# Kernel optimization log

Hardware: AMD Instinct MI355X
Metric: run time of the kernel (lower is better)

The kernel has to match this reference:

```python
import jax, jax.numpy as jnp
import numpy as np

NEG_INF = -1e9  # stand-in for -INF in masked_fill


def setup_inputs() -> dict:
    key = jax.random.key(0)
    k1, k2, k3 = jax.random.split(key, 3)
    B, S, D = 32, 8192, 512
    query = jax.random.normal(k1, (B, D), dtype=jnp.float32)
    key_t = jax.random.normal(k2, (B, S, D), dtype=jnp.float32)
    value = jax.random.normal(k3, (B, S, D), dtype=jnp.float32)
    mask = jnp.ones((B, 1, S), dtype=jnp.int32)
    return {"query": query, "key": key_t, "value": value, "mask": mask}


def reference(query, key, value, mask):
    # score: [B,1,S] = query [B,D] . key^T [B,D,S]
    score = jnp.einsum('bd,bsd->bs', query, key)[:, None, :]
    score = jnp.where(mask == 0, NEG_INF, score)
    probability = jax.nn.softmax(score, axis=-1)          # [B,1,S]
    out = jnp.einsum('bqs,bsd->bqd', probability, value)  # [B,1,D]
    return out[:, 0, :]                                   # squeeze(1) -> [B,D]
```

## Files before the change

### kernel.cpp

```cpp
#include <hip/hip_runtime.h>
#include <cstddef>

#define BATCH 32
#define SEQ   8192
#define DIM   512
#define NEG_INF_F (-1e9f)

#define NCHUNK 64
#define SCHUNK (SEQ / NCHUNK)

__global__ __launch_bounds__(256) void scores_kernel(
    const float* __restrict__ q, const float* __restrict__ k,
    const int* __restrict__ mask, float* __restrict__ score) {
  const int wave = threadIdx.x >> 6;
  const int lane = threadIdx.x & 63;
  const size_t row = (size_t)blockIdx.x * 4 + wave;
  const int b = (int)(row >> 13);
  const int s = (int)(row & (SEQ - 1));

  const float4* __restrict__ krow = (const float4*)(k + row * DIM);
  const float4* __restrict__ qrow = (const float4*)(q + (size_t)b * DIM);

  const int i0 = lane * 2;
  float4 k0 = krow[i0];
  float4 k1 = krow[i0 + 1];
  float4 q0 = qrow[i0];
  float4 q1 = qrow[i0 + 1];

  float d = k0.x * q0.x + k0.y * q0.y + k0.z * q0.z + k0.w * q0.w
          + k1.x * q1.x + k1.y * q1.y + k1.z * q1.z + k1.w * q1.w;

  #pragma unroll
  for (int off = 32; off > 0; off >>= 1) d += __shfl_down(d, off, 64);

  if (lane == 0) {
    float sc = (mask[(size_t)b * SEQ + s] == 0) ? NEG_INF_F : d;
    score[row] = sc;
  }
}

__global__ __launch_bounds__(256) void softmax_kernel(float* __restrict__ score) {
  __shared__ float red[4];
  const int b = blockIdx.x;
  float* __restrict__ sc = score + (size_t)b * SEQ;
  const int tid = threadIdx.x;

  float vals[SEQ / 256];
  float lmax = -3.0e38f;
  #pragma unroll
  for (int i = 0; i < SEQ / 256; ++i) {
    vals[i] = sc[tid + i * 256];
    lmax = fmaxf(lmax, vals[i]);
  }
  #pragma unroll
  for (int off = 32; off > 0; off >>= 1)
    lmax = fmaxf(lmax, __shfl_down(lmax, off, 64));
  if ((tid & 63) == 0) red[tid >> 6] = lmax;
  __syncthreads();
  const float m = fmaxf(fmaxf(red[0], red[1]), fmaxf(red[2], red[3]));
  __syncthreads();

  float lsum = 0.0f;
  #pragma unroll
  for (int i = 0; i < SEQ / 256; ++i) {
    vals[i] = __expf(vals[i] - m);
    lsum += vals[i];
  }
  #pragma unroll
  for (int off = 32; off > 0; off >>= 1) lsum += __shfl_down(lsum, off, 64);
  if ((tid & 63) == 0) red[tid >> 6] = lsum;
  __syncthreads();
  const float inv = 1.0f / (red[0] + red[1] + red[2] + red[3]);

  #pragma unroll
  for (int i = 0; i < SEQ / 256; ++i) sc[tid + i * 256] = vals[i] * inv;
}

__global__ __launch_bounds__(128) void pv_kernel(
    const float* __restrict__ p, const float* __restrict__ v,
    float* __restrict__ part) {
  __shared__ float pl[SCHUNK];
  const int b = blockIdx.x / NCHUNK;
  const int c = blockIdx.x % NCHUNK;
  const int tid = threadIdx.x;
  const int s0 = c * SCHUNK;

  pl[tid] = p[(size_t)b * SEQ + s0 + tid];
  __syncthreads();

  const float4* __restrict__ vbase =
      (const float4*)(v + ((size_t)b * SEQ + s0) * DIM);
  float4 acc = {0.f, 0.f, 0.f, 0.f};
  #pragma unroll 4
  for (int i = 0; i < SCHUNK; ++i) {
    float4 vv = vbase[(size_t)i * (DIM / 4) + tid];
    float ps = pl[i];
    acc.x += ps * vv.x;
    acc.y += ps * vv.y;
    acc.z += ps * vv.z;
    acc.w += ps * vv.w;
  }
  ((float4*)part)[((size_t)c * BATCH + b) * (DIM / 4) + tid] = acc;
}

__global__ __launch_bounds__(256) void reduce_kernel(
    const float* __restrict__ part, float* __restrict__ out) {
  const int idx = blockIdx.x * 256 + threadIdx.x;
  const float4* __restrict__ p4 = (const float4*)part;
  float4 acc = {0.f, 0.f, 0.f, 0.f};
  #pragma unroll 8
  for (int c = 0; c < NCHUNK; ++c) {
    float4 t = p4[(size_t)c * (BATCH * DIM / 4) + idx];
    acc.x += t.x; acc.y += t.y; acc.z += t.z; acc.w += t.w;
  }
  ((float4*)out)[idx] = acc;
}

extern "C" void kernel_launch(void* const* d_in, const int* in_sizes, int n_in,
                              void* d_out, int out_size, void* d_ws, size_t ws_size,
                              hipStream_t stream) {
  const float* q    = (const float*)d_in[0];
  const float* k    = (const float*)d_in[1];
  const float* v    = (const float*)d_in[2];
  const int*   mask = (const int*)d_in[3];
  float* out = (float*)d_out;

  float* score = (float*)d_ws;
  float* part  = score + (size_t)BATCH * SEQ;

  scores_kernel<<<BATCH * SEQ / 4, 256, 0, stream>>>(q, k, mask, score);
  softmax_kernel<<<BATCH, 256, 0, stream>>>(score);
  pv_kernel<<<BATCH * NCHUNK, 128, 0, stream>>>(score, v, part);
  reduce_kernel<<<BATCH * DIM / 4 / 256, 256, 0, stream>>>(part, out);
}
```

Before: 975.1 us.

## Fuse scores, softmax and PV into split-K flash-decode kernel with rescaled reduction

Replaces the four-kernel pipeline (scores, global softmax, PV, reduce) with one fused per-chunk kernel and a small final reduction. Each block computes its chunk's scores, a local max, exp weights and a partial sum, then accumulates P·V, writing the partial output plus the chunk max and sum. The final kernel rescales the partials with exp(m_c - m) and normalizes, as in flash-decoding. This removes the score round trip and two launches and overlaps K and V streaming within a block. The cost is fewer, heavier blocks (2048 of 256 threads), with serialized phases inside each block.

```diff
diff --git a/kernel.cpp b/kernel.cpp
--- a/kernel.cpp
+++ b/kernel.cpp
@@ -9,111 +9,119 @@
 #define NCHUNK 64
 #define SCHUNK (SEQ / NCHUNK)
 
-__global__ __launch_bounds__(256) void scores_kernel(
+__global__ __launch_bounds__(256) void fused_chunk_kernel(
     const float* __restrict__ q, const float* __restrict__ k,
-    const int* __restrict__ mask, float* __restrict__ score) {
-  const int wave = threadIdx.x >> 6;
-  const int lane = threadIdx.x & 63;
-  const size_t row = (size_t)blockIdx.x * 4 + wave;
-  const int b = (int)(row >> 13);
-  const int s = (int)(row & (SEQ - 1));
+    const float* __restrict__ v, const int* __restrict__ mask,
+    float* __restrict__ part,
+    float* __restrict__ mpart,
+    float* __restrict__ lpart) {
+  __shared__ float sc[SCHUNK];
+  __shared__ float wsm[SCHUNK];
+  __shared__ float4 vred[DIM / 4];
 
-  const float4* __restrict__ krow = (const float4*)(k + row * DIM);
-  const float4* __restrict__ qrow = (const float4*)(q + (size_t)b * DIM);
+  const int tid  = threadIdx.x;
+  const int wave = tid >> 6;
+  const int lane = tid & 63;
+  const int b  = blockIdx.x >> 6;
+  const int c  = blockIdx.x & (NCHUNK - 1);
+  const int s0 = c * SCHUNK;
 
-  const int i0 = lane * 2;
-  float4 k0 = krow[i0];
-  float4 k1 = krow[i0 + 1];
-  float4 q0 = qrow[i0];
-  float4 q1 = qrow[i0 + 1];
+  const float4* __restrict__ q4 = (const float4*)(q + (size_t)b * DIM);
+  const float4 q0 = q4[lane];
+  const float4 q1 = q4[lane + 64];
 
-  float d = k0.x * q0.x + k0.y * q0.y + k0.z * q0.z + k0.w * q0.w
-          + k1.x * q1.x + k1.y * q1.y + k1.z * q1.z + k1.w * q1.w;
+  const float4* __restrict__ k4 =
+      (const float4*)(k + ((size_t)b * SEQ + s0) * DIM);
 
+  #pragma unroll 2
+  for (int r = wave; r < SCHUNK; r += 4) {
+    const float4* __restrict__ krow = k4 + (size_t)r * (DIM / 4);
+    float4 k0 = krow[lane];
+    float4 k1 = krow[lane + 64];
+    float d = k0.x * q0.x + k0.y * q0.y + k0.z * q0.z + k0.w * q0.w
+            + k1.x * q1.x + k1.y * q1.y + k1.z * q1.z + k1.w * q1.w;
+    #pragma unroll
+    for (int off = 32; off > 0; off >>= 1) d += __shfl_down(d, off, 64);
+    if (lane == 0) {
+      int mk = mask[(size_t)b * SEQ + s0 + r];
+      sc[r] = mk ? d : NEG_INF_F;
+    }
+  }
+  __syncthreads();
+
+  const float x0 = sc[lane];
+  const float x1 = sc[lane + 64];
+  float m = fmaxf(x0, x1);
   #pragma unroll
-  for (int off = 32; off > 0; off >>= 1) d += __shfl_down(d, off, 64);
+  for (int off = 32; off > 0; off >>= 1)
+    m = fmaxf(m, __shfl_xor(m, off, 64));
 
-  if (lane == 0) {
-    float sc = (mask[(size_t)b * SEQ + s] == 0) ? NEG_INF_F : d;
-    score[row] = sc;
+  const float w0 = __expf(x0 - m);
+  const float w1 = __expf(x1 - m);
+  if (wave == 0) { wsm[lane] = w0; wsm[lane + 64] = w1; }
+
+  float ls = w0 + w1;
+  #pragma unroll
+  for (int off = 32; off > 0; off >>= 1) ls += __shfl_xor(ls, off, 64);
+
+  if (tid == 0) {
+    mpart[(size_t)c * BATCH + b] = m;
+    lpart[(size_t)c * BATCH + b] = ls;
+  }
+  __syncthreads();
+
+  const int cf = tid & 127;
+  const int h  = tid >> 7;
+  const float4* __restrict__ v4 =
+      (const float4*)(v + ((size_t)b * SEQ + s0) * DIM);
+
+  float4 acc = {0.f, 0.f, 0.f, 0.f};
+  #pragma unroll 4
+  for (int i = 0; i < SCHUNK / 2; ++i) {
+    const int r = 2 * i + h;
+    const float w = wsm[r];
+    float4 vv = v4[(size_t)r * (DIM / 4) + cf];
+    acc.x += w * vv.x;
+    acc.y += w * vv.y;
+    acc.z += w * vv.z;
+    acc.w += w * vv.w;
+  }
+  if (h == 1) vred[cf] = acc;
+  __syncthreads();
+  if (h == 0) {
+    float4 o = vred[cf];
+    acc.x += o.x; acc.y += o.y; acc.z += o.z; acc.w += o.w;
+    ((float4*)part)[((size_t)c * BATCH + b) * (DIM / 4) + cf] = acc;
   }
 }
 
-__global__ __launch_bounds__(256) void softmax_kernel(float* __restrict__ score) {
-  __shared__ float red[4];
+__global__ __launch_bounds__(128) void final_reduce_kernel(
+    const float* __restrict__ part, const float* __restrict__ mpart,
+    const float* __restrict__ lpart, float* __restrict__ out) {
   const int b = blockIdx.x;
-  float* __restrict__ sc = score + (size_t)b * SEQ;
-  const int tid = threadIdx.x;
+  const int t = threadIdx.x;
 
-  float vals[SEQ / 256];
-  float lmax = -3.0e38f;
+  float m = -3.0e38f;
   #pragma unroll
-  for (int i = 0; i < SEQ / 256; ++i) {
-    vals[i] = sc[tid + i * 256];
-    lmax = fmaxf(lmax, vals[i]);
-  }
-  #pragma unroll
-  for (int off = 32; off > 0; off >>= 1)
-    lmax = fmaxf(lmax, __shfl_down(lmax, off, 64));
-  if ((tid & 63) == 0) red[tid >> 6] = lmax;
-  __syncthreads();
-  const float m = fmaxf(fmaxf(red[0], red[1]), fmaxf(red[2], red[3]));
-  __syncthreads();
+  for (int c = 0; c < NCHUNK; ++c)
+    m = fmaxf(m, mpart[(size_t)c * BATCH + b]);
 
-  float lsum = 0.0f;
-  #pragma unroll
-  for (int i = 0; i < SEQ / 256; ++i) {
-    vals[i] = __expf(vals[i] - m);
-    lsum += vals[i];
-  }
-  #pragma unroll
-  for (int off = 32; off > 0; off >>= 1) lsum += __shfl_down(lsum, off, 64);
-  if ((tid & 63) == 0) red[tid >> 6] = lsum;
-  __syncthreads();
-  const float inv = 1.0f / (red[0] + red[1] + red[2] + red[3]);
-
-  #pragma unroll
-  for (int i = 0; i < SEQ / 256; ++i) sc[tid + i * 256] = vals[i] * inv;
-}
-
-__global__ __launch_bounds__(128) void pv_kernel(
-    const float* __restrict__ p, const float* __restrict__ v,
-    float* __restrict__ part) {
-  __shared__ float pl[SCHUNK];
-  const int b = blockIdx.x / NCHUNK;
-  const int c = blockIdx.x % NCHUNK;
-  const int tid = threadIdx.x;
-  const int s0 = c * SCHUNK;
-
-  pl[tid] = p[(size_t)b * SEQ + s0 + tid];
-  __syncthreads();
-
-  const float4* __restrict__ vbase =
-      (const float4*)(v + ((size_t)b * SEQ + s0) * DIM);
+  float L = 0.f;
   float4 acc = {0.f, 0.f, 0.f, 0.f};
   #pragma unroll 4
-  for (int i = 0; i < SCHUNK; ++i) {
-    float4 vv = vbase[(size_t)i * (DIM / 4) + tid];
-    float ps = pl[i];
-    acc.x += ps * vv.x;
-    acc.y += ps * vv.y;
-    acc.z += ps * vv.z;
-    acc.w += ps * vv.w;
+  for (int c = 0; c < NCHUNK; ++c) {
+    const float w = __expf(mpart[(size_t)c * BATCH + b] - m);
+    L += w * lpart[(size_t)c * BATCH + b];
+    float4 p = ((const float4*)part)[((size_t)c * BATCH + b) * (DIM / 4) + t];
+    acc.x += w * p.x;
+    acc.y += w * p.y;
+    acc.z += w * p.z;
+    acc.w += w * p.w;
   }
-  ((float4*)part)[((size_t)c * BATCH + b) * (DIM / 4) + tid] = acc;
-}
-
-__global__ __launch_bounds__(256) void reduce_kernel(
-    const float* __restrict__ part, float* __restrict__ out) {
-  const int idx = blockIdx.x * 256 + threadIdx.x;
-  const float4* __restrict__ p4 = (const float4*)part;
-  float4 acc = {0.f, 0.f, 0.f, 0.f};
-  #pragma unroll 8
-  for (int c = 0; c < NCHUNK; ++c) {
-    float4 t = p4[(size_t)c * (BATCH * DIM / 4) + idx];
-    acc.x += t.x; acc.y += t.y; acc.z += t.z; acc.w += t.w;
-  }
-  ((float4*)out)[idx] = acc;
+  const float inv = 1.0f / L;
+  float4 o;
+  o.x = acc.x * inv; o.y = acc.y * inv; o.z = acc.z * inv; o.w = acc.w * inv;
+  ((float4*)out)[(size_t)b * (DIM / 4) + t] = o;
 }
 
 extern "C" void kernel_launch(void* const* d_in, const int* in_sizes, int n_in,
@@ -125,11 +133,11 @@
   const int*   mask = (const int*)d_in[3];
   float* out = (float*)d_out;
 
-  float* score = (float*)d_ws;
-  float* part  = score + (size_t)BATCH * SEQ;
+  float* part  = (float*)d_ws;
+  float* mpart = part + (size_t)NCHUNK * BATCH * DIM;
+  float* lpart = mpart + (size_t)NCHUNK * BATCH;
 
-  scores_kernel<<<BATCH * SEQ / 4, 256, 0, stream>>>(q, k, mask, score);
-  softmax_kernel<<<BATCH, 256, 0, stream>>>(score);
-  pv_kernel<<<BATCH * NCHUNK, 128, 0, stream>>>(score, v, part);
-  reduce_kernel<<<BATCH * DIM / 4 / 256, 256, 0, stream>>>(part, out);
+  fused_chunk_kernel<<<BATCH * NCHUNK, 256, 0, stream>>>(
+      q, k, v, mask, part, mpart, lpart);
+  final_reduce_kernel<<<BATCH, 128, 0, stream>>>(part, mpart, lpart, out);
 }
```

Result: no change. 974.4 us (-0.1%).
